# Kernel optimization log

Measured on AMD Instinct MI355X. Metric: run time of the kernel, lower is better.

Reference implementation:

```python
import jax, jax.numpy as jnp
import numpy as np

B, DZ, DY, DX = 2, 200, 200, 100   # batch, voxel grid
N = 200000                          # active input voxels
C_IN, C_MID, C_OUT = 16, 64, 32
K = 27                              # 3x3x3 kernel offsets
EPS = 1e-5


def _pad_per_k(kid, a_in, a_out, pad_in, pad_out):
    # pack ragged per-offset pair lists into dense [K, Pmax] with dummy padding
    counts = np.bincount(kid, minlength=K)
    P = int(counts.max())
    I = np.full((K, P), pad_in, np.int32)
    O = np.full((K, P), pad_out, np.int32)
    order = np.argsort(kid, kind='stable')
    ks = kid[order]
    starts = np.cumsum(counts) - counts
    pos = np.arange(kid.size) - starts[ks]
    I[ks, pos] = a_in[order]
    O[ks, pos] = a_out[order]
    return I, O


def _build_structure(seed=0):
    # spconv-style indice-pair generation (rulebook) in numpy
    rng = np.random.default_rng(seed)
    lin = rng.choice(B * DZ * DY * DX, size=N, replace=False)
    b, r = np.divmod(lin, DZ * DY * DX)
    z, r = np.divmod(r, DY * DX)
    y, x = np.divmod(r, DX)
    coords = np.stack([b, z, y, x], 1)
    offs = np.stack(np.meshgrid(*[np.arange(3)] * 3, indexing='ij'), -1).reshape(K, 3)
    od = np.array([(DZ - 3) // 2 + 1, (DY - 3) // 2 + 1, (DX - 3) // 2 + 1])
    # stage 1: SparseConv3d k=3 s=2 p=0 -> output site o iff i = 2*o + k
    oc = coords[:, None, 1:] - offs[None]            # (N, 27, 3)
    valid = (oc >= 0).all(-1) & (oc % 2 == 0).all(-1)
    oq = oc // 2
    valid &= (oq < od).all(-1)
    pi, pk = np.nonzero(valid)
    oz, oy, ox = oq[pi, pk, 0], oq[pi, pk, 1], oq[pi, pk, 2]
    olin = ((coords[pi, 0] * od[0] + oz) * od[1] + oy) * od[2] + ox
    uniq, inv = np.unique(olin, return_inverse=True)
    n1 = int(len(uniq))
    p1_in, p1_out = _pad_per_k(pk, pi.astype(np.int32), inv.astype(np.int32), N, n1)
    # stage 2: SubMConv3d k=3 on stage-1 sites (output sites == input sites)
    c1b, r = np.divmod(uniq, od[0] * od[1] * od[2])
    c1z, r = np.divmod(r, od[1] * od[2])
    c1y, c1x = np.divmod(r, od[2])
    coords1 = np.stack([c1b, c1z, c1y, c1x], 1)
    nc = coords1[:, None, 1:] + (offs - 1)[None]     # (n1, 27, 3) neighbor coords
    valid2 = (nc >= 0).all(-1) & (nc < od).all(-1)
    pj, pk2 = np.nonzero(valid2)
    nl = ((coords1[pj, 0] * od[0] + nc[pj, pk2, 0]) * od[1] + nc[pj, pk2, 1]) * od[2] + nc[pj, pk2, 2]
    pos = np.minimum(np.searchsorted(uniq, nl), n1 - 1)
    ok = uniq[pos] == nl
    p2_in, p2_out = _pad_per_k(pk2[ok], pos[ok].astype(np.int32), pj[ok].astype(np.int32), n1, n1)
    return p1_in, p1_out, p2_in, p2_out, n1


def _ggs(feats, W, pin, pout, n_out):
    # gather-gemm-scatter sparse conv; pin padded with feats.shape[0], pout with n_out
    fpad = jnp.concatenate([feats, jnp.zeros((1, feats.shape[1]), feats.dtype)], 0)
    out = jnp.zeros((n_out + 1, W.shape[2]), feats.dtype)
    for k in range(W.shape[0]):
        out = out.at[pout[k]].add(fpad[pin[k]] @ W[k])
    return out[:n_out]


def _bn_relu(x, g, b):
    # BatchNorm1d (training-mode batch stats, biased var) + ReLU
    m = x.mean(0)
    v = x.var(0)
    return jax.nn.relu((x - m) * jax.lax.rsqrt(v + EPS) * g + b)


def setup_inputs():
    p1_in, p1_out, p2_in, p2_out, n1 = _build_structure(0)
    key = jax.random.key(0)
    k1, k2, k3, k4 = jax.random.split(key, 4)
    return {
        'feats': jax.random.normal(k1, (N, C_IN), jnp.float32),
        'W1': jax.random.normal(k2, (K, C_IN, C_MID), jnp.float32) * 0.05,
        'gamma1': jnp.ones((C_MID,), jnp.float32),
        'beta1': jnp.zeros((C_MID,), jnp.float32),
        'W2': jax.random.normal(k3, (K, C_MID, C_MID), jnp.float32) * 0.05,
        'gamma2': jnp.ones((C_MID,), jnp.float32),
        'beta2': jnp.zeros((C_MID,), jnp.float32),
        'W3': jax.random.normal(k4, (K, C_MID, C_OUT), jnp.float32) * 0.05,
        'p1_in': jnp.asarray(p1_in), 'p1_out': jnp.asarray(p1_out),
        'p2_in': jnp.asarray(p2_in), 'p2_out': jnp.asarray(p2_out),
        'n1': n1,
    }


def reference(feats, W1, gamma1, beta1, W2, gamma2, beta2, W3, p1_in, p1_out, p2_in, p2_out, n1):
    x = _ggs(feats, W1, p1_in, p1_out, n1)                        # SparseConv3d(Cin,64,3,2)
    x = _bn_relu(x, gamma1, beta1)
    x = _bn_relu(_ggs(x, W2, p2_in, p2_out, n1), gamma2, beta2)   # SubMConv3d(64,64,3)
    return _ggs(x, W3, p1_out, p1_in, N)                          # SparseInverseConv3d: pairs swapped
```

## Files before the change

kernel.cpp:

```cpp
#include <hip/hip_runtime.h>
#include <hip/hip_bf16.h>

typedef __bf16 bf16x8 __attribute__((ext_vector_type(8)));
typedef float f32x4 __attribute__((ext_vector_type(4)));

__device__ __forceinline__ unsigned short f2bf(float x) {
  union { float f; unsigned int u; } v; v.f = x;
  unsigned int r = (v.u + 0x7FFFu + ((v.u >> 16) & 1u)) >> 16;
  return (unsigned short)r;
}
__device__ __forceinline__ float bf2f(unsigned short u) {
  union { unsigned int u; float f; } v; v.u = ((unsigned int)u) << 16;
  return v.f;
}

__global__ void cvt_feats_kernel(const float* __restrict__ f, unsigned short* __restrict__ fb, int n16) {
  int t = blockIdx.x * 256 + threadIdx.x;
  if (t >= n16) return;
  fb[t] = f2bf(f[t]);
}

__global__ void pack_w_kernel(const float* __restrict__ W, unsigned short* __restrict__ Wp,
                              int CI, int CO, int NT, int KK) {
  int t = blockIdx.x * 256 + threadIdx.x;
  int total = 27 * NT * KK * 512;
  if (t >= total) return;
  int j = t & 7, l = (t >> 3) & 63;
  int g = t >> 9;
  int kk = g % KK; g /= KK;
  int nt = g % NT; int k = g / NT;
  int kg = kk * 32 + ((l >> 4) * 8) + j;
  int c = nt * 16 + (l & 15);
  float v = (kg < CI) ? W[((size_t)k * CI + kg) * CO + c] : 0.0f;
  Wp[t] = f2bf(v);
}

__global__ void pack_w_paired_kernel(const float* __restrict__ W, unsigned short* __restrict__ Wp,
                                     int CO, int NT) {
  int t = blockIdx.x * 256 + threadIdx.x;
  int total = 14 * NT * 512;
  if (t >= total) return;
  int j = t & 7, l = (t >> 3) & 63;
  int g = t >> 9;
  int nt = g % NT; int gp = g / NT;
  int kg = ((l >> 4) * 8) + j;
  int k = 2 * gp + (kg >= 16 ? 1 : 0);
  int ci = kg & 15;
  int c = nt * 16 + (l & 15);
  float v = (k <= 26) ? W[((size_t)k * 16 + ci) * CO + c] : 0.0f;
  Wp[t] = f2bf(v);
}

__global__ void build_table_kernel(const int* __restrict__ pin, const int* __restrict__ pout,
                                   int P, int maxo, int* __restrict__ tab,
                                   const int* __restrict__ n_ptr, int n_cap) {
  int p = blockIdx.x * 256 + threadIdx.x;
  if (p >= P) return;
  int k = blockIdx.y;
  int n = n_cap;
  if (n_ptr) { int nv = n_ptr[0]; if (nv < n) n = nv; }
  size_t e = (size_t)k * P + p;
  int o = pout[e];
  if (o < n) tab[(size_t)k * maxo + o] = pin[e];
}

#define LDTAB(KC_, TARR) do {                                                    \
    int _k2 = PAIRED ? (2 * (KC_) + klb) : (KC_);                                \
    int _kc = _k2 > 26 ? 26 : _k2;                                               \
    _Pragma("unroll") for (int _m = 0; _m < MT; ++_m) {                          \
      int _t = tab[(size_t)_kc * maxo + rowm[_m]];                               \
      TARR[_m] = (PAIRED && _k2 > 26) ? -1 : _t;                                 \
    }                                                                            \
  } while (0)

#define ISSUE_A(AB, TARR, D) do {                                                \
    if (SKIP) {                                                                  \
      bool _anyv = (TARR[0] >= 0);                                               \
      _Pragma("unroll") for (int _m = 1; _m < MT; ++_m)                          \
        _anyv = _anyv || (TARR[_m] >= 0);                                        \
      D = (__ballot(_anyv) != 0ull);                                             \
    }                                                                            \
    _Pragma("unroll") for (int _m = 0; _m < MT; ++_m) {                          \
      const unsigned short* _s = Xb + (size_t)(TARR[_m] < 0 ? zrow : TARR[_m]) * ROWS + loff; \
      _Pragma("unroll") for (int kk = 0; kk < KK; ++kk)                          \
        AB[_m][kk] = *reinterpret_cast<const bf16x8*>(_s + kk * 32);             \
    }                                                                            \
  } while (0)

#define STAGE_B2(KB, PB) do {                                                    \
    _Pragma("unroll") for (int _s = 0; _s < 2; ++_s) {                           \
      if ((KB) + _s <= MAXK) {                                                   \
        size_t _kb = (size_t)((KB) + _s) * (size_t)SZ;                           \
        _Pragma("unroll") for (int _j = 0; _j < PER; ++_j) {                     \
          int _c = w * PER + _j;                                                 \
          const unsigned char* _gp = WpB + _kb + (size_t)_c * 1024 + (size_t)l * 16; \
          __builtin_amdgcn_global_load_lds(                                      \
              (const __attribute__((address_space(1))) void*)_gp,                \
              (__attribute__((address_space(3))) void*)((PB) + _s * SZ + _c * 1024), 16, 0, 0); \
        }                                                                        \
      }                                                                          \
    }                                                                            \
  } while (0)

#define STEP_CORE(BCUR, AB, D) do {                                              \
    if (!SKIP || (D)) {                                                          \
      _Pragma("unroll") for (int kk = 0; kk < KK; ++kk)                          \
        _Pragma("unroll") for (int nt = 0; nt < NT; ++nt) {                      \
          bf16x8 b = *reinterpret_cast<const bf16x8*>(&(BCUR)[(nt * KK + kk) * 1024 + l * 16]); \
          _Pragma("unroll") for (int _m = 0; _m < MT; ++_m)                      \
            acc[_m][nt] = __builtin_amdgcn_mfma_f32_16x16x32_bf16(AB[_m][kk], b, acc[_m][nt], 0, 0, 0); \
        }                                                                        \
    }                                                                            \
  } while (0)

#define GROUP_BARRIER() do {                                                     \
    __builtin_amdgcn_sched_barrier(0);                                           \
    asm volatile("s_waitcnt vmcnt(%0)" :: "n"(NWAIT) : "memory");                \
    __builtin_amdgcn_sched_barrier(0);                                           \
    __builtin_amdgcn_s_barrier();                                                \
  } while (0)

template<int KK, int NT, int MT, bool SKIP, bool PAIRED>
__global__ __launch_bounds__(256, 4) void conv_mfma_kernel(
    const unsigned short* __restrict__ Xb, const unsigned short* __restrict__ Wp,
    const int* __restrict__ tab, int maxo, int zrow,
    const int* __restrict__ n_ptr, int n_cap,
    unsigned short* __restrict__ outb, float* __restrict__ outf,
    float* __restrict__ stats_out) {
  const int CO = NT * 16;
  const int ROWS = PAIRED ? 16 : KK * 32;
  const int RPW = 16 * MT;
  constexpr int PER = (KK * NT) / 4;
  constexpr int SZ = KK * NT * 1024;
  constexpr int MAXK = PAIRED ? 13 : 26;
  constexpr int GROUPS = PAIRED ? 6 : 13;
  constexpr int NWAIT = 2 * MT * KK + 2 * MT;

  __shared__ __align__(16) unsigned char Blds[2][2][SZ];
  __shared__ float bs[2][64];

  int bid = blockIdx.x;
  {
    int nwg = gridDim.x;
    int q = nwg >> 3, r = nwg & 7;
    int xcd = bid & 7, orig = bid >> 3;
    bid = (xcd < r ? xcd * (q + 1) : r * (q + 1) + (xcd - r) * q) + orig;
  }

  int w = threadIdx.x >> 6, l = threadIdx.x & 63;
  int n_rows = n_cap;
  if (n_ptr) { int nv = n_ptr[0]; if (nv < n_rows) n_rows = nv; }
  if (bid * 4 * RPW >= n_rows) return;
  int lr = l & 15, lg = l >> 4;
  int klb = lg >> 1;
  int loff = PAIRED ? (lg & 1) * 8 : lg * 8;
  int wbase = bid * 4 * RPW + w * RPW;

  if (stats_out && threadIdx.x < 128)
    bs[threadIdx.x >> 6][threadIdx.x & 63] = 0.f;

  int rowm[MT];
#pragma unroll
  for (int m = 0; m < MT; ++m) {
    int r = wbase + m * 16 + lr;
    rowm[m] = r < n_rows ? r : (n_rows - 1);
  }

  const unsigned char* WpB = (const unsigned char*)Wp;

  f32x4 acc[MT][NT] = {};
  bf16x8 a0[MT][KK], a1[MT][KK];
  int tE[MT], tO[MT];
  bool dE = true, dO = true;

  LDTAB(0, tE);
  LDTAB(1, tO);
  STAGE_B2(0, &Blds[0][0][0]);
  __builtin_amdgcn_sched_barrier(0);
  ISSUE_A(a0, tE, dE);
  ISSUE_A(a1, tO, dO);
  LDTAB(2, tE);
  LDTAB(3, tO);
  GROUP_BARRIER();

#pragma unroll 1
  for (int g = 0; g < GROUPS; ++g) {
    int kb = g * 2;
    unsigned char* bc = &Blds[g & 1][0][0];
    unsigned char* bn = &Blds[(g + 1) & 1][0][0];
    STAGE_B2(kb + 2, bn);
    __builtin_amdgcn_sched_barrier(0);
    STEP_CORE(bc + 0 * SZ, a0, dE); ISSUE_A(a0, tE, dE); LDTAB(kb + 4, tE);
    STEP_CORE(bc + 1 * SZ, a1, dO); ISSUE_A(a1, tO, dO); LDTAB(kb + 5, tO);
    GROUP_BARRIER();
  }
  {
    unsigned char* bt = &Blds[GROUPS & 1][0][0];
    STEP_CORE(bt + 0 * SZ, a0, dE);
    if (PAIRED) STEP_CORE(bt + 1 * SZ, a1, dO);
  }

  float sS[NT] = {}, sQ[NT] = {};
#pragma unroll
  for (int mt = 0; mt < MT; ++mt) {
    int r0 = wbase + mt * 16 + lg * 4;
#pragma unroll
    for (int rr = 0; rr < 4; ++rr) {
      int row = r0 + rr;
      if (row < n_rows) {
#pragma unroll
        for (int nt = 0; nt < NT; ++nt) {
          float v = acc[mt][nt][rr];
          size_t off = (size_t)row * CO + nt * 16 + lr;
          if (outf) outf[off] = v;
          else outb[off] = f2bf(v);
          sS[nt] += v; sQ[nt] += v * v;
        }
      }
    }
  }
  if (stats_out) {
#pragma unroll
    for (int nt = 0; nt < NT; ++nt) {
      sS[nt] += __shfl_xor(sS[nt], 16); sS[nt] += __shfl_xor(sS[nt], 32);
      sQ[nt] += __shfl_xor(sQ[nt], 16); sQ[nt] += __shfl_xor(sQ[nt], 32);
    }
    if (l < 16) {
#pragma unroll
      for (int nt = 0; nt < NT; ++nt) {
        atomicAdd(&bs[0][nt * 16 + lr], sS[nt]);
        atomicAdd(&bs[1][nt * 16 + lr], sQ[nt]);
      }
    }
    __syncthreads();
    if (threadIdx.x < 128) {
      int h = threadIdx.x >> 6, c = threadIdx.x & 63;
      atomicAdd(&stats_out[h * 64 + c], bs[h][c]);
    }
  }
}

__global__ void bn_apply_kernel(unsigned short* __restrict__ xb,
                                const int* __restrict__ n_ptr, int n_cap,
                                const float* __restrict__ stats,
                                const float* __restrict__ gamma, const float* __restrict__ beta) {
  int c = threadIdx.x & 63, q = threadIdx.x >> 6;
  int n = n_ptr[0]; if (n > n_cap) n = n_cap;
  float inv_n = 1.f / (float)n;
  float m = stats[c] * inv_n;
  float var = stats[64 + c] * inv_n - m * m;
  float sc = gamma[c] * rsqrtf(var + 1e-5f);
  float sh = beta[c] - m * sc;
  for (int r = blockIdx.x * 4 + q; r < n; r += gridDim.x * 4) {
    size_t off = (size_t)r * 64 + c;
    float v = bf2f(xb[off]) * sc + sh;
    xb[off] = f2bf(v > 0.f ? v : 0.f);
  }
}

extern "C" void kernel_launch(void* const* d_in, const int* in_sizes, int n_in,
                              void* d_out, int out_size, void* d_ws, size_t ws_size,
                              hipStream_t stream) {
  const float* feats  = (const float*)d_in[0];
  const float* W1     = (const float*)d_in[1];
  const float* g1     = (const float*)d_in[2];
  const float* b1     = (const float*)d_in[3];
  const float* W2     = (const float*)d_in[4];
  const float* g2     = (const float*)d_in[5];
  const float* b2     = (const float*)d_in[6];
  const float* W3     = (const float*)d_in[7];
  const int* p1_in    = (const int*)d_in[8];
  const int* p1_out   = (const int*)d_in[9];
  const int* p2_in    = (const int*)d_in[10];
  const int* p2_out   = (const int*)d_in[11];
  const int* d_n1     = (const int*)d_in[12];
  float* out = (float*)d_out;

  const int N  = in_sizes[0] / 16;
  const int P1 = in_sizes[8] / 27;
  const int P2 = in_sizes[10] / 27;
  long KP1 = in_sizes[8];
  int n1b = (int)(KP1 < 980100 ? KP1 : 980100);
  int maxo = n1b > N ? n1b : N;

  char* p = (char*)d_ws;
  auto alloc = [&](size_t bytes) -> char* {
    char* r = p; p += (bytes + 255) & ~(size_t)255; return r;
  };
  unsigned short* featsb = (unsigned short*)alloc((size_t)(N + 1) * 16 * 2);
  unsigned short* x1b    = (unsigned short*)alloc((size_t)(n1b + 1) * 64 * 2);
  unsigned short* x2b    = (unsigned short*)alloc((size_t)(n1b + 1) * 64 * 2);
  unsigned short* W1p    = (unsigned short*)alloc((size_t)14 * 4 * 512 * 2);
  unsigned short* W2p    = (unsigned short*)alloc((size_t)27 * 4 * 2 * 512 * 2);
  unsigned short* W3p    = (unsigned short*)alloc((size_t)27 * 2 * 2 * 512 * 2);
  int*   tab   = (int*)alloc((size_t)maxo * 27 * 4);
  float* stats = (float*)alloc(256 * 4);
  if ((size_t)(p - (char*)d_ws) > ws_size) return;

  hipMemsetAsync(featsb + (size_t)N * 16, 0, 16 * 2, stream);
  hipMemsetAsync(x1b + (size_t)n1b * 64, 0, 64 * 2, stream);
  hipMemsetAsync(x2b + (size_t)n1b * 64, 0, 64 * 2, stream);
  hipMemsetAsync(stats, 0, 256 * 4, stream);

  cvt_feats_kernel<<<(N * 16 + 255) / 256, 256, 0, stream>>>(feats, featsb, N * 16);
  pack_w_paired_kernel<<<(14 * 4 * 512 + 255) / 256, 256, 0, stream>>>(W1, W1p, 64, 4);
  pack_w_kernel<<<(27 * 4 * 2 * 512 + 255) / 256, 256, 0, stream>>>(W2, W2p, 64, 64, 4, 2);
  pack_w_kernel<<<(27 * 2 * 2 * 512 + 255) / 256, 256, 0, stream>>>(W3, W3p, 64, 32, 2, 2);

  hipMemsetAsync(tab, 0xFF, (size_t)n1b * 27 * 4, stream);
  build_table_kernel<<<dim3((P1 + 255) / 256, 27), 256, 0, stream>>>(
      p1_in, p1_out, P1, n1b, tab, d_n1, n1b);
  conv_mfma_kernel<1, 4, 2, true, true><<<(n1b + 127) / 128, 256, 0, stream>>>(
      featsb, W1p, tab, n1b, N, d_n1, n1b, x1b, nullptr, stats);
  bn_apply_kernel<<<2048, 256, 0, stream>>>(x1b, d_n1, n1b, stats, g1, b1);

  hipMemsetAsync(tab, 0xFF, (size_t)n1b * 27 * 4, stream);
  build_table_kernel<<<dim3((P2 + 255) / 256, 27), 256, 0, stream>>>(
      p2_in, p2_out, P2, n1b, tab, d_n1, n1b);
  conv_mfma_kernel<2, 4, 2, false, false><<<(n1b + 127) / 128, 256, 0, stream>>>(
      x1b, W2p, tab, n1b, n1b, d_n1, n1b, x2b, nullptr, stats + 128);
  bn_apply_kernel<<<2048, 256, 0, stream>>>(x2b, d_n1, n1b, stats + 128, g2, b2);

  hipMemsetAsync(tab, 0xFF, (size_t)N * 27 * 4, stream);
  build_table_kernel<<<dim3((P1 + 255) / 256, 27), 256, 0, stream>>>(
      p1_out, p1_in, P1, N, tab, nullptr, N);
  conv_mfma_kernel<2, 2, 2, true, false><<<(N + 127) / 128, 256, 0, stream>>>(
      x2b, W3p, tab, N, n1b, nullptr, N, nullptr, out, nullptr);
}
```

Measured before the change: 592.0 us.

## Fuse BatchNorm+ReLU into the consumer conv's gathered A operand

Removes the two standalone bn_apply passes and instead applies scale/shift/ReLU to each gathered bf16 A fragment inside the next convolution kernel, with per-lane BN coefficients computed once at kernel start. Missing neighbors (zero rows) are forced to zero after the affine transform so padding stays correct. This drops a full read-modify-write over the intermediate activations but recomputes BN on every gathered row (about 27 times per row), adding VALU work and register pressure (scl/shl arrays) in the MFMA loop.

```diff
diff --git a/kernel.cpp b/kernel.cpp
--- a/kernel.cpp
+++ b/kernel.cpp
@@ -73,7 +73,7 @@
     }                                                                            \
   } while (0)
 
-#define ISSUE_A(AB, TARR, D) do {                                                \
+#define ISSUE_A(AB, ZARR, TARR, D) do {                                          \
     if (SKIP) {                                                                  \
       bool _anyv = (TARR[0] >= 0);                                               \
       _Pragma("unroll") for (int _m = 1; _m < MT; ++_m)                          \
@@ -81,6 +81,7 @@
       D = (__ballot(_anyv) != 0ull);                                             \
     }                                                                            \
     _Pragma("unroll") for (int _m = 0; _m < MT; ++_m) {                          \
+      ZARR[_m] = (TARR[_m] < 0);                                                 \
       const unsigned short* _s = Xb + (size_t)(TARR[_m] < 0 ? zrow : TARR[_m]) * ROWS + loff; \
       _Pragma("unroll") for (int kk = 0; kk < KK; ++kk)                          \
         AB[_m][kk] = *reinterpret_cast<const bf16x8*>(_s + kk * 32);             \
@@ -102,8 +103,21 @@
     }                                                                            \
   } while (0)
 
-#define STEP_CORE(BCUR, AB, D) do {                                              \
+#define STEP_CORE(BCUR, AB, ZB, D) do {                                          \
     if (!SKIP || (D)) {                                                          \
+      if (BNIN) {                                                                \
+        _Pragma("unroll") for (int _m = 0; _m < MT; ++_m)                        \
+          _Pragma("unroll") for (int kk = 0; kk < KK; ++kk) {                    \
+            bf16x8 _a = AB[_m][kk];                                              \
+            _Pragma("unroll") for (int _j = 0; _j < 8; ++_j) {                   \
+              float _v = (float)_a[_j];                                          \
+              _v = _v * scl[kk][_j] + shl[kk][_j];                               \
+              _v = _v > 0.f ? _v : 0.f;                                          \
+              _a[_j] = (__bf16)(ZB[_m] ? 0.f : _v);                              \
+            }                                                                    \
+            AB[_m][kk] = _a;                                                     \
+          }                                                                      \
+      }                                                                          \
       _Pragma("unroll") for (int kk = 0; kk < KK; ++kk)                          \
         _Pragma("unroll") for (int nt = 0; nt < NT; ++nt) {                      \
           bf16x8 b = *reinterpret_cast<const bf16x8*>(&(BCUR)[(nt * KK + kk) * 1024 + l * 16]); \
@@ -120,13 +134,15 @@
     __builtin_amdgcn_s_barrier();                                                \
   } while (0)
 
-template<int KK, int NT, int MT, bool SKIP, bool PAIRED>
+template<int KK, int NT, int MT, bool SKIP, bool PAIRED, bool BNIN>
 __global__ __launch_bounds__(256, 4) void conv_mfma_kernel(
     const unsigned short* __restrict__ Xb, const unsigned short* __restrict__ Wp,
     const int* __restrict__ tab, int maxo, int zrow,
     const int* __restrict__ n_ptr, int n_cap,
     unsigned short* __restrict__ outb, float* __restrict__ outf,
-    float* __restrict__ stats_out) {
+    float* __restrict__ stats_out,
+    const float* __restrict__ bn_stats, const float* __restrict__ bn_gamma,
+    const float* __restrict__ bn_beta, const int* __restrict__ bn_nptr, int bn_ncap) {
   const int CO = NT * 16;
   const int ROWS = PAIRED ? 16 : KK * 32;
   const int RPW = 16 * MT;
@@ -159,6 +175,23 @@
   if (stats_out && threadIdx.x < 128)
     bs[threadIdx.x >> 6][threadIdx.x & 63] = 0.f;
 
+  float scl[KK][8], shl[KK][8];
+  if (BNIN) {
+    int bn_n = bn_nptr[0]; if (bn_n > bn_ncap) bn_n = bn_ncap;
+    float inv_n = 1.f / (float)bn_n;
+#pragma unroll
+    for (int kk = 0; kk < KK; ++kk)
+#pragma unroll
+      for (int j = 0; j < 8; ++j) {
+        int c = kk * 32 + lg * 8 + j;
+        float m = bn_stats[c] * inv_n;
+        float var = bn_stats[64 + c] * inv_n - m * m;
+        float s = bn_gamma[c] * rsqrtf(var + 1e-5f);
+        scl[kk][j] = s; shl[kk][j] = bn_beta[c] - m * s;
+      }
+  }
+  __builtin_amdgcn_sched_barrier(0);
+
   int rowm[MT];
 #pragma unroll
   for (int m = 0; m < MT; ++m) {
@@ -170,6 +203,7 @@
 
   f32x4 acc[MT][NT] = {};
   bf16x8 a0[MT][KK], a1[MT][KK];
+  bool z0[MT], z1[MT];
   int tE[MT], tO[MT];
   bool dE = true, dO = true;
 
@@ -177,8 +211,8 @@
   LDTAB(1, tO);
   STAGE_B2(0, &Blds[0][0][0]);
   __builtin_amdgcn_sched_barrier(0);
-  ISSUE_A(a0, tE, dE);
-  ISSUE_A(a1, tO, dO);
+  ISSUE_A(a0, z0, tE, dE);
+  ISSUE_A(a1, z1, tO, dO);
   LDTAB(2, tE);
   LDTAB(3, tO);
   GROUP_BARRIER();
@@ -187,17 +221,17 @@
   for (int g = 0; g < GROUPS; ++g) {
     int kb = g * 2;
     unsigned char* bc = &Blds[g & 1][0][0];
-    unsigned char* bn = &Blds[(g + 1) & 1][0][0];
-    STAGE_B2(kb + 2, bn);
+    unsigned char* bn_ = &Blds[(g + 1) & 1][0][0];
+    STAGE_B2(kb + 2, bn_);
     __builtin_amdgcn_sched_barrier(0);
-    STEP_CORE(bc + 0 * SZ, a0, dE); ISSUE_A(a0, tE, dE); LDTAB(kb + 4, tE);
-    STEP_CORE(bc + 1 * SZ, a1, dO); ISSUE_A(a1, tO, dO); LDTAB(kb + 5, tO);
+    STEP_CORE(bc + 0 * SZ, a0, z0, dE); ISSUE_A(a0, z0, tE, dE); LDTAB(kb + 4, tE);
+    STEP_CORE(bc + 1 * SZ, a1, z1, dO); ISSUE_A(a1, z1, tO, dO); LDTAB(kb + 5, tO);
     GROUP_BARRIER();
   }
   {
     unsigned char* bt = &Blds[GROUPS & 1][0][0];
-    STEP_CORE(bt + 0 * SZ, a0, dE);
-    if (PAIRED) STEP_CORE(bt + 1 * SZ, a1, dO);
+    STEP_CORE(bt + 0 * SZ, a0, z0, dE);
+    if (PAIRED) STEP_CORE(bt + 1 * SZ, a1, z1, dO);
   }
 
   float sS[NT] = {}, sQ[NT] = {};
@@ -237,24 +271,6 @@
       int h = threadIdx.x >> 6, c = threadIdx.x & 63;
       atomicAdd(&stats_out[h * 64 + c], bs[h][c]);
     }
-  }
-}
-
-__global__ void bn_apply_kernel(unsigned short* __restrict__ xb,
-                                const int* __restrict__ n_ptr, int n_cap,
-                                const float* __restrict__ stats,
-                                const float* __restrict__ gamma, const float* __restrict__ beta) {
-  int c = threadIdx.x & 63, q = threadIdx.x >> 6;
-  int n = n_ptr[0]; if (n > n_cap) n = n_cap;
-  float inv_n = 1.f / (float)n;
-  float m = stats[c] * inv_n;
-  float var = stats[64 + c] * inv_n - m * m;
-  float sc = gamma[c] * rsqrtf(var + 1e-5f);
-  float sh = beta[c] - m * sc;
-  for (int r = blockIdx.x * 4 + q; r < n; r += gridDim.x * 4) {
-    size_t off = (size_t)r * 64 + c;
-    float v = bf2f(xb[off]) * sc + sh;
-    xb[off] = f2bf(v > 0.f ? v : 0.f);
   }
 }
 
@@ -310,20 +326,21 @@
   hipMemsetAsync(tab, 0xFF, (size_t)n1b * 27 * 4, stream);
   build_table_kernel<<<dim3((P1 + 255) / 256, 27), 256, 0, stream>>>(
       p1_in, p1_out, P1, n1b, tab, d_n1, n1b);
-  conv_mfma_kernel<1, 4, 2, true, true><<<(n1b + 127) / 128, 256, 0, stream>>>(
-      featsb, W1p, tab, n1b, N, d_n1, n1b, x1b, nullptr, stats);
-  bn_apply_kernel<<<2048, 256, 0, stream>>>(x1b, d_n1, n1b, stats, g1, b1);
+  conv_mfma_kernel<1, 4, 2, true, true, false><<<(n1b + 127) / 128, 256, 0, stream>>>(
+      featsb, W1p, tab, n1b, N, d_n1, n1b, x1b, nullptr, stats,
+      nullptr, nullptr, nullptr, nullptr, 0);
 
   hipMemsetAsync(tab, 0xFF, (size_t)n1b * 27 * 4, stream);
   build_table_kernel<<<dim3((P2 + 255) / 256, 27), 256, 0, stream>>>(
       p2_in, p2_out, P2, n1b, tab, d_n1, n1b);
-  conv_mfma_kernel<2, 4, 2, false, false><<<(n1b + 127) / 128, 256, 0, stream>>>(
-      x1b, W2p, tab, n1b, n1b, d_n1, n1b, x2b, nullptr, stats + 128);
-  bn_apply_kernel<<<2048, 256, 0, stream>>>(x2b, d_n1, n1b, stats + 128, g2, b2);
+  conv_mfma_kernel<2, 4, 2, false, false, true><<<(n1b + 127) / 128, 256, 0, stream>>>(
+      x1b, W2p, tab, n1b, n1b, d_n1, n1b, x2b, nullptr, stats + 128,
+      stats, g1, b1, d_n1, n1b);
 
   hipMemsetAsync(tab, 0xFF, (size_t)N * 27 * 4, stream);
   build_table_kernel<<<dim3((P1 + 255) / 256, 27), 256, 0, stream>>>(
       p1_out, p1_in, P1, N, tab, nullptr, N);
-  conv_mfma_kernel<2, 2, 2, true, false><<<(N + 127) / 128, 256, 0, stream>>>(
-      x2b, W3p, tab, N, n1b, nullptr, N, nullptr, out, nullptr);
-}
+  conv_mfma_kernel<2, 2, 2, true, false, true><<<(N + 127) / 128, 256, 0, stream>>>(
+      x2b, W3p, tab, N, n1b, nullptr, N, nullptr, out, nullptr,
+      stats + 128, g2, b2, d_n1, n1b);
+}
```

Result: slower. 642.3 us (+8.5%).
